# Kernel tuning notes

Measured on AMD Instinct MI355X. Metric: run time of the kernel, lower is better.

The kernel has to match this reference:

```python
import jax, jax.numpy as jnp
import numpy as np


def setup_inputs() -> dict:
    key = jax.random.key(0)
    k1, k2 = jax.random.split(key)
    B, C, H, W = 32, 256, 64, 64
    data = jax.random.normal(k1, (B, C, H, W), dtype=jnp.float32)
    offset = jax.random.normal(k2, (B, 2, H, W), dtype=jnp.float32)
    trans_std = jnp.float32(0.005)  # learned scalar Parameter
    return {"data": data, "offset": offset, "trans_std": trans_std}


def reference(data, offset, trans_std):
    """Offset-driven bilinear interpolation sampling + global average pooling.

    data:   [B, C, H, W]
    offset: [B, 2, H, W]  (dy, dx) displacement field, scaled by trans_std
    Returns pooled features [B, C].
    """
    B, C, H, W = data.shape
    ts = jnp.clip(trans_std, 0.001, 0.01)  # forward clamps trans_std to [0.001, 0.01]

    # sampling coordinates: base grid + scaled offsets (offsets normalized by H/W)
    ii = jnp.arange(H, dtype=data.dtype)[:, None]   # [H,1]
    jj = jnp.arange(W, dtype=data.dtype)[None, :]   # [1,W]
    y = jnp.clip(ii + ts * offset[:, 0] * H, 0.0, H - 1)  # [B,H,W]
    x = jnp.clip(jj + ts * offset[:, 1] * W, 0.0, W - 1)  # [B,H,W]

    y0 = jnp.clip(jnp.floor(y).astype(jnp.int32), 0, H - 2)
    x0 = jnp.clip(jnp.floor(x).astype(jnp.int32), 0, W - 2)
    y1 = y0 + 1
    x1 = x0 + 1
    wy = y - y0.astype(data.dtype)  # [B,H,W] in [0,1]
    wx = x - x0.astype(data.dtype)

    def sample_one(d, yy0, yy1, xx0, xx1):
        # d: [C,H,W]; index maps: [H,W] -> gathered [C,H,W]
        v00 = d[:, yy0, xx0]
        v01 = d[:, yy0, xx1]
        v10 = d[:, yy1, xx0]
        v11 = d[:, yy1, xx1]
        return v00, v01, v10, v11

    v00, v01, v10, v11 = jax.vmap(sample_one)(data, y0, y1, x0, x1)  # each [B,C,H,W]

    wy_ = wy[:, None]  # broadcast over channels -> [B,1,H,W]
    wx_ = wx[:, None]
    sampled = ((1 - wy_) * (1 - wx_) * v00 + (1 - wy_) * wx_ * v01
               + wy_ * (1 - wx_) * v10 + wy_ * wx_ * v11)  # [B,C,H,W]

    # pooling: global average over spatial locations -> [B,C]
    return jnp.mean(sampled, axis=(2, 3))
```

## Files before the change

### kernel.cpp

```cpp
#include <hip/hip_runtime.h>
#include <stdint.h>

#define BATCH 32
#define CHAN  256
#define HGT   64
#define WID   64
#define HW    4096
#define GPB   8
#define CPB   32

typedef float v4f __attribute__((ext_vector_type(4)));

#define GLOAD8(B0,B1,B2,B3,B4,B5,B6,B7, P0, P1)                       \
    asm volatile(                                                      \
        "global_load_dwordx4 %0, %8, off\n\t"                          \
        "global_load_dwordx4 %1, %8, off offset:1024\n\t"              \
        "global_load_dwordx4 %2, %8, off offset:2048\n\t"              \
        "global_load_dwordx4 %3, %8, off offset:3072\n\t"              \
        "global_load_dwordx4 %4, %9, off\n\t"                          \
        "global_load_dwordx4 %5, %9, off offset:1024\n\t"              \
        "global_load_dwordx4 %6, %9, off offset:2048\n\t"              \
        "global_load_dwordx4 %7, %9, off offset:3072"                  \
        : "=&v"(B0), "=&v"(B1), "=&v"(B2), "=&v"(B3),                  \
          "=&v"(B4), "=&v"(B5), "=&v"(B6), "=&v"(B7)                   \
        : "v"(P0), "v"(P1)                                             \
        : "memory")

#define WAITVM(N)                                                      \
    asm volatile("s_waitcnt vmcnt(" #N ")" ::: "memory");              \
    __builtin_amdgcn_sched_barrier(0)

#define FMA4(S, AV, DV)                                                \
    S = fmaf((AV).x, (DV).x, S); S = fmaf((AV).y, (DV).y, S);          \
    S = fmaf((AV).z, (DV).z, S); S = fmaf((AV).w, (DV).w, S)

#define DRAIN8(B0,B1,B2,B3,B4,B5,B6,B7, HP, S0,S1,S2,S3)               \
    { const float4 a0_ = *reinterpret_cast<const float4*>((HP) + 0*256); FMA4(S0, a0_, B0); \
      const float4 a1_ = *reinterpret_cast<const float4*>((HP) + 1*256); FMA4(S1, a1_, B1); \
      const float4 a2_ = *reinterpret_cast<const float4*>((HP) + 2*256); FMA4(S2, a2_, B2); \
      const float4 a3_ = *reinterpret_cast<const float4*>((HP) + 3*256); FMA4(S3, a3_, B3); \
      const float4 a4_ = *reinterpret_cast<const float4*>((HP) + 4*256); FMA4(S0, a4_, B4); \
      const float4 a5_ = *reinterpret_cast<const float4*>((HP) + 5*256); FMA4(S1, a5_, B5); \
      const float4 a6_ = *reinterpret_cast<const float4*>((HP) + 6*256); FMA4(S2, a6_, B6); \
      const float4 a7_ = *reinterpret_cast<const float4*>((HP) + 7*256); FMA4(S3, a7_, B7); }

__global__ __launch_bounds__(1024) void fused_bilinear_pool(
        const float* __restrict__ data,
        const float* __restrict__ offset,
        const float* __restrict__ ts_ptr,
        float* __restrict__ out)
{
    const int blk  = blockIdx.x;
    const int b    = blk >> 3;
    const int g    = blk & 7;
    const int tid  = threadIdx.x;
    const int w    = tid >> 6;
    const int lane = tid & 63;

    __shared__ float acc[HW];

    acc[tid]        = 0.0f;
    acc[tid + 1024] = 0.0f;
    acc[tid + 2048] = 0.0f;
    acc[tid + 3072] = 0.0f;
    __syncthreads();

    const float* off_y = offset + (size_t)b * 2 * HW;
    const float* off_x = off_y + HW;
    const float4 dy4 = *reinterpret_cast<const float4*>(off_y + tid * 4);
    const float4 dx4 = *reinterpret_cast<const float4*>(off_x + tid * 4);

    float ts = ts_ptr[0];
    ts = fminf(fmaxf(ts, 0.001f), 0.01f);

    {
        const int i  = tid >> 4;
        const int j0 = (tid << 2) & 63;
        const float dys[4] = {dy4.x, dy4.y, dy4.z, dy4.w};
        const float dxs[4] = {dx4.x, dx4.y, dx4.z, dx4.w};
        #pragma unroll
        for (int e = 0; e < 4; ++e) {
            float y = fminf(fmaxf((float)i        + ts * dys[e] * 64.0f, 0.0f), 63.0f);
            float x = fminf(fmaxf((float)(j0 + e) + ts * dxs[e] * 64.0f, 0.0f), 63.0f);
            int y0 = (int)floorf(y); y0 = min(max(y0, 0), HGT - 2);
            int x0 = (int)floorf(x); x0 = min(max(x0, 0), WID - 2);
            const float wy = y - (float)y0;
            const float wx = x - (float)x0;
            const int base = (y0 << 6) + x0;
            atomicAdd(&acc[base],           (1.0f - wy) * (1.0f - wx));
            atomicAdd(&acc[base + 1],       (1.0f - wy) * wx);
            atomicAdd(&acc[base + WID],     wy * (1.0f - wx));
            atomicAdd(&acc[base + WID + 1], wy * wx);
        }
    }
    __syncthreads();

    const int c0 = g * CPB;
    const float* p0 = data + ((size_t)b * CHAN + c0 + w) * HW + lane * 4;
    const float* p1 = p0 + 16 * HW;

    const float* hp0 = acc + lane * 4;
    const float* hp1 = acc + 2048 + lane * 4;

    v4f A0,A1,A2,A3,A4,A5,A6,A7;
    v4f B0,B1,B2,B3,B4,B5,B6,B7;

    GLOAD8(A0,A1,A2,A3,A4,A5,A6,A7, p0,        p0 + 1024);
    GLOAD8(B0,B1,B2,B3,B4,B5,B6,B7, p0 + 2048, p0 + 3072);

    float s0=0.f,s1=0.f,s2=0.f,s3=0.f;
    float t0=0.f,t1=0.f,t2=0.f,t3=0.f;

    WAITVM(8);
    DRAIN8(A0,A1,A2,A3,A4,A5,A6,A7, hp0, s0,s1,s2,s3);
    GLOAD8(A0,A1,A2,A3,A4,A5,A6,A7, p1,        p1 + 1024);

    WAITVM(8);
    DRAIN8(B0,B1,B2,B3,B4,B5,B6,B7, hp1, s0,s1,s2,s3);
    GLOAD8(B0,B1,B2,B3,B4,B5,B6,B7, p1 + 2048, p1 + 3072);

    WAITVM(8);
    DRAIN8(A0,A1,A2,A3,A4,A5,A6,A7, hp0, t0,t1,t2,t3);

    WAITVM(0);
    DRAIN8(B0,B1,B2,B3,B4,B5,B6,B7, hp1, t0,t1,t2,t3);

    float sum0 = (s0 + s1) + (s2 + s3);
    float sum1 = (t0 + t1) + (t2 + t3);

    #pragma unroll
    for (int off = 32; off > 0; off >>= 1) {
        sum0 += __shfl_down(sum0, off, 64);
        sum1 += __shfl_down(sum1, off, 64);
    }

    if (lane == 0) {
        const float s = 1.0f / (float)HW;
        out[(b << 8) + c0 + w]      = sum0 * s;
        out[(b << 8) + c0 + w + 16] = sum1 * s;
    }
}

extern "C" void kernel_launch(void* const* d_in, const int* in_sizes, int n_in,
                              void* d_out, int out_size, void* d_ws, size_t ws_size,
                              hipStream_t stream) {
    const float* data   = (const float*)d_in[0];
    const float* offset = (const float*)d_in[1];
    const float* ts     = (const float*)d_in[2];

    float* out = (float*)d_out;
    (void)d_ws; (void)ws_size;

    fused_bilinear_pool<<<BATCH * GPB, 1024, 0, stream>>>(data, offset, ts, out);
}
```

Before: 214.9 us.

## Use 512-thread blocks and prefetch data loads before building weight map

Halves the block to 512 threads, so each wave now handles 4 channels and each thread processes 8 offset pixels when building the shared bilinear weight histogram. The first batch of data loads is issued before the atomic weight-map construction, so global memory latency overlaps with the LDS atomics. Launch bounds allow two blocks per CU. Per-thread register use grows with 32 live vector buffers, and there is more serial atomic work per thread.

Result: faster. 202.6 us (-5.7%).

```diff
diff --git a/kernel.cpp b/kernel.cpp
--- a/kernel.cpp
+++ b/kernel.cpp
@@ -26,6 +26,11 @@
         : "v"(P0), "v"(P1)                                             \
         : "memory")
 
+#define GLOADP(R, P)                                                   \
+    GLOAD8(R##0,R##1,R##2,R##3,R##4,R##5,R##6,R##7, (P), (P) + 1024);  \
+    GLOAD8(R##8,R##9,R##10,R##11,R##12,R##13,R##14,R##15,              \
+           (P) + 2048, (P) + 3072)
+
 #define WAITVM(N)                                                      \
     asm volatile("s_waitcnt vmcnt(" #N ")" ::: "memory");              \
     __builtin_amdgcn_sched_barrier(0)
@@ -44,7 +49,13 @@
       const float4 a6_ = *reinterpret_cast<const float4*>((HP) + 6*256); FMA4(S2, a6_, B6); \
       const float4 a7_ = *reinterpret_cast<const float4*>((HP) + 7*256); FMA4(S3, a7_, B7); }
 
-__global__ __launch_bounds__(1024) void fused_bilinear_pool(
+#define DRAINP(R, HP0, HP1, OUTF)                                      \
+    { float s0_=0.f,s1_=0.f,s2_=0.f,s3_=0.f;                           \
+      DRAIN8(R##0,R##1,R##2,R##3,R##4,R##5,R##6,R##7, HP0, s0_,s1_,s2_,s3_); \
+      DRAIN8(R##8,R##9,R##10,R##11,R##12,R##13,R##14,R##15, HP1, s0_,s1_,s2_,s3_); \
+      OUTF = (s0_ + s1_) + (s2_ + s3_); }
+
+__global__ __launch_bounds__(512, 2) void fused_bilinear_pool(
         const float* __restrict__ data,
         const float* __restrict__ offset,
         const float* __restrict__ ts_ptr,
@@ -59,27 +70,47 @@
 
     __shared__ float acc[HW];
 
-    acc[tid]        = 0.0f;
-    acc[tid + 1024] = 0.0f;
-    acc[tid + 2048] = 0.0f;
-    acc[tid + 3072] = 0.0f;
-    __syncthreads();
-
-    const float* off_y = offset + (size_t)b * 2 * HW;
-    const float* off_x = off_y + HW;
-    const float4 dy4 = *reinterpret_cast<const float4*>(off_y + tid * 4);
-    const float4 dx4 = *reinterpret_cast<const float4*>(off_x + tid * 4);
-
     float ts = ts_ptr[0];
     ts = fminf(fmaxf(ts, 0.001f), 0.01f);
 
+    #pragma unroll
+    for (int z = 0; z < 8; ++z) acc[tid + z * 512] = 0.0f;
+    __syncthreads();
+
+    const float* off_y = offset + (size_t)b * 2 * HW + tid * 8;
+    const float* off_x = off_y + HW;
+    v4f dy4a, dy4b, dx4a, dx4b;
+    asm volatile(
+        "global_load_dwordx4 %0, %4, off\n\t"
+        "global_load_dwordx4 %1, %4, off offset:16\n\t"
+        "global_load_dwordx4 %2, %5, off\n\t"
+        "global_load_dwordx4 %3, %5, off offset:16"
+        : "=&v"(dy4a), "=&v"(dy4b), "=&v"(dx4a), "=&v"(dx4b)
+        : "v"(off_y), "v"(off_x)
+        : "memory");
+
+    const int c0 = g * CPB;
+    const float* p0 = data + ((size_t)b * CHAN + c0 + w) * HW + lane * 4;
+    const float* p1 = p0 + 8 * HW;
+    const float* p2 = p0 + 16 * HW;
+    const float* p3 = p0 + 24 * HW;
+
+    v4f A0,A1,A2,A3,A4,A5,A6,A7,A8,A9,A10,A11,A12,A13,A14,A15;
+    v4f B0,B1,B2,B3,B4,B5,B6,B7,B8,B9,B10,B11,B12,B13,B14,B15;
+
+    GLOADP(A, p0);
+
+    WAITVM(16);
+
     {
-        const int i  = tid >> 4;
-        const int j0 = (tid << 2) & 63;
-        const float dys[4] = {dy4.x, dy4.y, dy4.z, dy4.w};
-        const float dxs[4] = {dx4.x, dx4.y, dx4.z, dx4.w};
+        const int i  = tid >> 3;
+        const int j0 = (tid & 7) * 8;
+        const float dys[8] = {dy4a.x, dy4a.y, dy4a.z, dy4a.w,
+                              dy4b.x, dy4b.y, dy4b.z, dy4b.w};
+        const float dxs[8] = {dx4a.x, dx4a.y, dx4a.z, dx4a.w,
+                              dx4b.x, dx4b.y, dx4b.z, dx4b.w};
         #pragma unroll
-        for (int e = 0; e < 4; ++e) {
+        for (int e = 0; e < 8; ++e) {
             float y = fminf(fmaxf((float)i        + ts * dys[e] * 64.0f, 0.0f), 63.0f);
             float x = fminf(fmaxf((float)(j0 + e) + ts * dxs[e] * 64.0f, 0.0f), 63.0f);
             int y0 = (int)floorf(y); y0 = min(max(y0, 0), HGT - 2);
@@ -95,49 +126,37 @@
     }
     __syncthreads();
 
-    const int c0 = g * CPB;
-    const float* p0 = data + ((size_t)b * CHAN + c0 + w) * HW + lane * 4;
-    const float* p1 = p0 + 16 * HW;
-
     const float* hp0 = acc + lane * 4;
     const float* hp1 = acc + 2048 + lane * 4;
 
-    v4f A0,A1,A2,A3,A4,A5,A6,A7;
-    v4f B0,B1,B2,B3,B4,B5,B6,B7;
+    float r0, r1, r2, r3;
 
-    GLOAD8(A0,A1,A2,A3,A4,A5,A6,A7, p0,        p0 + 1024);
-    GLOAD8(B0,B1,B2,B3,B4,B5,B6,B7, p0 + 2048, p0 + 3072);
-
-    float s0=0.f,s1=0.f,s2=0.f,s3=0.f;
-    float t0=0.f,t1=0.f,t2=0.f,t3=0.f;
-
-    WAITVM(8);
-    DRAIN8(A0,A1,A2,A3,A4,A5,A6,A7, hp0, s0,s1,s2,s3);
-    GLOAD8(A0,A1,A2,A3,A4,A5,A6,A7, p1,        p1 + 1024);
-
-    WAITVM(8);
-    DRAIN8(B0,B1,B2,B3,B4,B5,B6,B7, hp1, s0,s1,s2,s3);
-    GLOAD8(B0,B1,B2,B3,B4,B5,B6,B7, p1 + 2048, p1 + 3072);
-
-    WAITVM(8);
-    DRAIN8(A0,A1,A2,A3,A4,A5,A6,A7, hp0, t0,t1,t2,t3);
-
+    GLOADP(B, p1);
+    DRAINP(A, hp0, hp1, r0);
+    GLOADP(A, p2);
+    WAITVM(16);
+    DRAINP(B, hp0, hp1, r1);
+    GLOADP(B, p3);
+    WAITVM(16);
+    DRAINP(A, hp0, hp1, r2);
     WAITVM(0);
-    DRAIN8(B0,B1,B2,B3,B4,B5,B6,B7, hp1, t0,t1,t2,t3);
-
-    float sum0 = (s0 + s1) + (s2 + s3);
-    float sum1 = (t0 + t1) + (t2 + t3);
+    DRAINP(B, hp0, hp1, r3);
 
     #pragma unroll
     for (int off = 32; off > 0; off >>= 1) {
-        sum0 += __shfl_down(sum0, off, 64);
-        sum1 += __shfl_down(sum1, off, 64);
+        r0 += __shfl_down(r0, off, 64);
+        r1 += __shfl_down(r1, off, 64);
+        r2 += __shfl_down(r2, off, 64);
+        r3 += __shfl_down(r3, off, 64);
     }
 
     if (lane == 0) {
         const float s = 1.0f / (float)HW;
-        out[(b << 8) + c0 + w]      = sum0 * s;
-        out[(b << 8) + c0 + w + 16] = sum1 * s;
+        float* ob = out + (b << 8) + c0 + w;
+        ob[0]  = r0 * s;
+        ob[8]  = r1 * s;
+        ob[16] = r2 * s;
+        ob[24] = r3 * s;
     }
 }
 
@@ -151,5 +170,5 @@
     float* out = (float*)d_out;
     (void)d_ws; (void)ws_size;
 
-    fused_bilinear_pool<<<BATCH * GPB, 1024, 0, stream>>>(data, offset, ts, out);
+    fused_bilinear_pool<<<BATCH * GPB, 512, 0, stream>>>(data, offset, ts, out);
 }
```
